# Kernel tuning notes

Hardware: AMD Instinct MI355X
Metric: run time of the kernel (lower is better)

## Reference

```python
import jax, jax.numpy as jnp
import numpy as np

D_MODEL = 1024


def _n2_features(N_tokens):
    # N = token + 1; matrix rows (flattened, row-major) per original build_n2_matrix:
    # [ (N-1)^2, N-1, N,
    #   (N-1)^2, 2N,  -1,
    #   (N-1)^2, 0,   2(N-0.5),
    #   (N-1)^2, 2(N-0.5), 0 ]
    t = N_tokens.astype(jnp.float32)          # t = N - 1
    t2 = t * t                                # (N-1)^2
    z = jnp.zeros_like(t)
    neg1 = -jnp.ones_like(t)
    two_t_p1 = 2.0 * t + 1.0                  # 2*(N-0.5)
    feats = jnp.stack(
        [t2, t, t + 1.0,
         t2, 2.0 * t + 2.0, neg1,
         t2, z, two_t_p1,
         t2, two_t_p1, z],
        axis=-1,
    )                                          # [B, S, 12]
    return feats


def setup_inputs() -> dict:
    key = jax.random.key(0)
    k_tok, k_w, k_b = jax.random.split(key, 3)
    N_tokens = jax.random.randint(k_tok, (4, 8192), 0, 32000, dtype=jnp.int64)
    # nn.Linear(12, d_model): weight [d_model, 12], bias [d_model]
    bound = 1.0 / np.sqrt(12.0)
    W = jax.random.uniform(k_w, (D_MODEL, 12), jnp.float32, -bound, bound)
    b = jax.random.uniform(k_b, (D_MODEL,), jnp.float32, -bound, bound)
    return {"N_tokens": N_tokens, "W": W, "b": b}


def reference(N_tokens, W, b):
    feats = _n2_features(N_tokens)             # [B, S, 12]
    return jnp.einsum('bsf,df->bsd', feats, W) + b
```

## Files before the change

kernel.cpp:

```cpp
#include <hip/hip_runtime.h>

#define D_MODEL 1024
#define TPB_TOKENS 32

typedef float vfloat4 __attribute__((ext_vector_type(4)));

__global__ __launch_bounds__(256) void n2_embed_kernel(
    const int* __restrict__ toks,
    const float* __restrict__ W,
    const float* __restrict__ bias,
    float* __restrict__ out,
    int n_tokens)
{
    const int d0 = threadIdx.x * 4;

    float wv[48];
    const vfloat4* wp = (const vfloat4*)(W + (size_t)d0 * 12);
#pragma unroll
    for (int k = 0; k < 12; ++k)
        ((vfloat4*)wv)[k] = wp[k];

    const vfloat4 bb = *(const vfloat4*)(bias + d0);

    float A[4], B[4], C[4];
#pragma unroll
    for (int j = 0; j < 4; ++j) {
        const float* w = wv + j * 12;
        float w0 = w[0], w1 = w[1], w2 = w[2], w3 = w[3];
        float w4 = w[4], w5 = w[5], w6 = w[6];
        float w8 = w[8], w9 = w[9], w10 = w[10];
        A[j] = (w0 + w3) + (w6 + w9);
        B[j] = w1 + w2 + 2.0f * w4 + 2.0f * w8 + 2.0f * w10;
        C[j] = w2 + 2.0f * w4 - w5 + w8 + w10 + bb[j];
    }

    const int tok_begin = blockIdx.x * TPB_TOKENS;

    float tvals[TPB_TOKENS];
#pragma unroll
    for (int i = 0; i < TPB_TOKENS; ++i) {
        int tok = tok_begin + i;
        tvals[i] = (tok < n_tokens) ? (float)toks[tok] : 0.0f;
    }

#pragma unroll
    for (int i = 0; i < TPB_TOKENS; ++i) {
        int tok = tok_begin + i;
        if (tok >= n_tokens) break;
        float t = tvals[i];
        float t2 = t * t;
        vfloat4 o;
        o.x = fmaf(t2, A[0], fmaf(t, B[0], C[0]));
        o.y = fmaf(t2, A[1], fmaf(t, B[1], C[1]));
        o.z = fmaf(t2, A[2], fmaf(t, B[2], C[2]));
        o.w = fmaf(t2, A[3], fmaf(t, B[3], C[3]));
        *(vfloat4*)(out + (size_t)tok * D_MODEL + d0) = o;
    }
}

extern "C" void kernel_launch(void* const* d_in, const int* in_sizes, int n_in,
                              void* d_out, int out_size, void* d_ws, size_t ws_size,
                              hipStream_t stream) {
    const int* toks = (const int*)d_in[0];
    const float* W = (const float*)d_in[1];
    const float* bias = (const float*)d_in[2];
    float* out = (float*)d_out;

    int n_tokens = out_size / D_MODEL;
    int blocks = (n_tokens + TPB_TOKENS - 1) / TPB_TOKENS;

    n2_embed_kernel<<<blocks, 256, 0, stream>>>(toks, W, bias, out, n_tokens);
}
```

Measured before the change: 141.8 us.

## Interleave token assignment across blocks and halve tokens per block

Each block now handles tokens strided by the grid size instead of a contiguous run, so concurrently running blocks write adjacent output rows. Tokens per block drop to 16, doubling the block count, and launch bounds request 8 blocks per SM. Weight loads are split into per-row vector loads instead of one 48-float register array. The aim is better write locality and occupancy for a store-bound kernel, at the cost of fewer stores per block to amortize the weight setup over.

```diff
diff --git a/kernel.cpp b/kernel.cpp
--- a/kernel.cpp
+++ b/kernel.cpp
@@ -1,53 +1,49 @@
 #include <hip/hip_runtime.h>
 
 #define D_MODEL 1024
-#define TPB_TOKENS 32
+#define TPB_TOKENS 16
 
 typedef float vfloat4 __attribute__((ext_vector_type(4)));
 
-__global__ __launch_bounds__(256) void n2_embed_kernel(
+__global__ __launch_bounds__(256, 8) void n2_embed_kernel(
     const int* __restrict__ toks,
     const float* __restrict__ W,
     const float* __restrict__ bias,
     float* __restrict__ out,
-    int n_tokens)
+    int n_tokens,
+    int stride)
 {
     const int d0 = threadIdx.x * 4;
-
-    float wv[48];
-    const vfloat4* wp = (const vfloat4*)(W + (size_t)d0 * 12);
-#pragma unroll
-    for (int k = 0; k < 12; ++k)
-        ((vfloat4*)wv)[k] = wp[k];
 
     const vfloat4 bb = *(const vfloat4*)(bias + d0);
 
     float A[4], B[4], C[4];
 #pragma unroll
     for (int j = 0; j < 4; ++j) {
-        const float* w = wv + j * 12;
-        float w0 = w[0], w1 = w[1], w2 = w[2], w3 = w[3];
-        float w4 = w[4], w5 = w[5], w6 = w[6];
-        float w8 = w[8], w9 = w[9], w10 = w[10];
+        const vfloat4* wp = (const vfloat4*)(W + (size_t)(d0 + j) * 12);
+        vfloat4 wa = wp[0], wb = wp[1], wc = wp[2];
+        float w0 = wa.x, w1 = wa.y, w2 = wa.z, w3 = wa.w;
+        float w4 = wb.x, w5 = wb.y, w6 = wb.z;
+        float w8 = wc.x, w9 = wc.y, w10 = wc.z;
         A[j] = (w0 + w3) + (w6 + w9);
         B[j] = w1 + w2 + 2.0f * w4 + 2.0f * w8 + 2.0f * w10;
         C[j] = w2 + 2.0f * w4 - w5 + w8 + w10 + bb[j];
     }
 
-    const int tok_begin = blockIdx.x * TPB_TOKENS;
+    const int b = blockIdx.x;
 
-    float tvals[TPB_TOKENS];
+    float tv[TPB_TOKENS];
 #pragma unroll
-    for (int i = 0; i < TPB_TOKENS; ++i) {
-        int tok = tok_begin + i;
-        tvals[i] = (tok < n_tokens) ? (float)toks[tok] : 0.0f;
+    for (int k = 0; k < TPB_TOKENS; ++k) {
+        int tok = b + k * stride;
+        tv[k] = (tok < n_tokens) ? (float)toks[tok] : 0.0f;
     }
 
 #pragma unroll
-    for (int i = 0; i < TPB_TOKENS; ++i) {
-        int tok = tok_begin + i;
-        if (tok >= n_tokens) break;
-        float t = tvals[i];
+    for (int k = 0; k < TPB_TOKENS; ++k) {
+        int tok = b + k * stride;
+        if (tok >= n_tokens) continue;
+        float t = tv[k];
         float t2 = t * t;
         vfloat4 o;
         o.x = fmaf(t2, A[0], fmaf(t, B[0], C[0]));
@@ -69,5 +65,6 @@
     int n_tokens = out_size / D_MODEL;
     int blocks = (n_tokens + TPB_TOKENS - 1) / TPB_TOKENS;
 
-    n2_embed_kernel<<<blocks, 256, 0, stream>>>(toks, W, bias, out, n_tokens);
+    n2_embed_kernel<<<blocks, 256, 0, stream>>>(toks, W, bias, out,
+                                                n_tokens, blocks);
 }
```

After: 161.0 us. 13.5% more time.
